# Kernel tuning notes

Measured on AMD Instinct MI355X. Metric: run time of the kernel, lower is better.

Reference implementation:

```python
import jax, jax.numpy as jnp
import numpy as np

LOTRI2MAT = np.array([[0, 1, 3], [1, 2, 4], [3, 4, 5]])  # lower-tri 6-vec -> symmetric 3x3
MAT2LOTRI_I = np.array([0, 1, 1, 2, 2, 2])
MAT2LOTRI_J = np.array([0, 0, 1, 0, 1, 2])


def trilinear_warp_border(img, ddf):
    """MONAI Warp(mode='bilinear', padding_mode='border', align_corners=True).
    img: (B,C,H,W,D), ddf: (B,3,H,W,D) displacement in voxel units.
    Samples img at x + ddf(x), clamping coords to the volume (border padding).
    """
    B, C, H, W, D = img.shape
    base = jnp.stack(
        jnp.meshgrid(jnp.arange(H), jnp.arange(W), jnp.arange(D), indexing='ij'),
        axis=0,
    ).astype(img.dtype)  # (3,H,W,D)
    coords = ddf + base[None]  # (B,3,H,W,D)
    x = jnp.clip(coords[:, 0], 0.0, H - 1)
    y = jnp.clip(coords[:, 1], 0.0, W - 1)
    z = jnp.clip(coords[:, 2], 0.0, D - 1)

    x0f, y0f, z0f = jnp.floor(x), jnp.floor(y), jnp.floor(z)
    fx, fy, fz = x - x0f, y - y0f, z - z0f
    x0 = jnp.clip(x0f.astype(jnp.int32), 0, H - 1)
    y0 = jnp.clip(y0f.astype(jnp.int32), 0, W - 1)
    z0 = jnp.clip(z0f.astype(jnp.int32), 0, D - 1)
    x1 = jnp.minimum(x0 + 1, H - 1)
    y1 = jnp.minimum(y0 + 1, W - 1)
    z1 = jnp.minimum(z0 + 1, D - 1)

    def gather(img_b, xi, yi, zi):
        flat = (xi * W + yi) * D + zi  # (H,W,D)
        return img_b.reshape(C, -1)[:, flat.reshape(-1)].reshape(C, H, W, D)

    g = jax.vmap(gather)  # over batch

    out = jnp.zeros_like(img)
    for xi, wx in ((x0, 1.0 - fx), (x1, fx)):
        for yi, wy in ((y0, 1.0 - fy), (y1, fy)):
            for zi, wz in ((z0, 1.0 - fz), (z1, fz)):
                out = out + g(img, xi, yi, zi) * (wx * wy * wz)[:, None]
    return out


def jacobian_of_ddf(ddf):
    """J = I + du/dx via central differences (one-sided at boundaries).
    ddf: (B,3,H,W,D) -> (B,H,W,D,3,3) with J[...,i,j] = d u_i / d x_j + delta_ij."""
    grads = jnp.gradient(ddf, axis=(2, 3, 4))  # list over j of (B,3,H,W,D)
    J = jnp.stack(grads, axis=2)  # (B,3(i),3(j),H,W,D)
    J = J + jnp.eye(3, dtype=ddf.dtype)[None, :, :, None, None, None]
    return jnp.transpose(J, (0, 3, 4, 5, 1, 2))  # (B,H,W,D,3,3)


def setup_inputs() -> dict:
    key = jax.random.key(0)
    k1, k2 = jax.random.split(key)
    dti = jax.random.normal(k1, (2, 6, 64, 64, 64), dtype=jnp.float32)
    ddf = jax.random.normal(k2, (2, 3, 64, 64, 64), dtype=jnp.float32)
    return {"dti": dti, "ddf": ddf}


def reference(dti, ddf):
    b, _, h, w, d = dti.shape
    # 1) trilinear warp of the 6-channel lower-tri DTI
    dti_warped = trilinear_warp_border(dti, ddf)  # (B,6,H,W,D)
    # 2) lower-tri -> full symmetric 3x3, spatial-last
    M = dti_warped[:, LOTRI2MAT]                      # (B,3,3,H,W,D)
    M = jnp.transpose(M, (0, 3, 4, 5, 1, 2))          # (B,H,W,D,3,3)
    # 3) Jacobian of the deformation and its polar-decomposition rotation (finite strain)
    J = jacobian_of_ddf(ddf)                          # (B,H,W,D,3,3)
    U, _, Vh = jnp.linalg.svd(J, full_matrices=False)
    R = jnp.matmul(U, Vh)                             # orthogonal factor of J
    # 4) rotate tensors: R^T M R
    out = jnp.einsum('...ji,...jk,...kl->...il', R, M, R)
    # 5) back to lower-tri channel-first form
    out = jnp.transpose(out, (0, 4, 5, 1, 2, 3))      # (B,3,3,H,W,D)
    return out[:, MAT2LOTRI_I, MAT2LOTRI_J]           # (B,6,H,W,D)
```

## Files before the change

kernel.cpp:

```cpp
#include <hip/hip_runtime.h>

#define NVOX 262144
#define TOTAL (2 * NVOX)

typedef float f2u __attribute__((ext_vector_type(2), aligned(4)));

__global__ void zero_count(int* __restrict__ bad) {
    if (threadIdx.x == 0) bad[0] = 0;
}

__global__ __launch_bounds__(256)
void warp_main(const float* __restrict__ dti,
               const float* __restrict__ ddf,
               float* __restrict__ out,
               int* __restrict__ bad, int max_bad)
{
    const int idx = blockIdx.x * 256 + threadIdx.x;
    const int b = idx >> 18;
    const int r = idx & (NVOX - 1);
    const int x = r >> 12;
    const int y = (r >> 6) & 63;
    const int z = r & 63;

    const float* db = ddf + (size_t)b * 3 * NVOX;

    const float ux = db[r];
    const float uy = db[NVOX + r];
    const float uz = db[2 * NVOX + r];

    const float cx = fminf(fmaxf((float)x + ux, 0.0f), 63.0f);
    const float cy = fminf(fmaxf((float)y + uy, 0.0f), 63.0f);
    const float cz = fminf(fmaxf((float)z + uz, 0.0f), 63.0f);
    const float fx0 = floorf(cx), fy0 = floorf(cy), fz0 = floorf(cz);
    const float fx = cx - fx0, fy = cy - fy0, fz = cz - fz0;
    const int x0 = (int)fx0, y0 = (int)fy0, z0 = (int)fz0;
    const int x1 = min(x0 + 1, 63), y1 = min(y0 + 1, 63);

    const float gx = 1.0f - fx, gy = 1.0f - fy, gz = 1.0f - fz;
    const float q00 = gx * gy, q01 = gx * fy, q10 = fx * gy, q11 = fx * fy;

    const bool ztop = (z0 == 63);
    const int zb = ztop ? 62 : z0;
    const int p00 = (x0 * 64 + y0) * 64 + zb, p01 = (x0 * 64 + y1) * 64 + zb;
    const int p10 = (x1 * 64 + y0) * 64 + zb, p11 = (x1 * 64 + y1) * 64 + zb;

    const float* tb = dti + (size_t)b * 6 * NVOX;
    float m[6];
#pragma unroll
    for (int c = 0; c < 6; ++c) {
        const float* tc = tb + c * NVOX;
        const f2u v00 = *(const f2u*)(tc + p00);
        const f2u v01 = *(const f2u*)(tc + p01);
        const f2u v10 = *(const f2u*)(tc + p10);
        const f2u v11 = *(const f2u*)(tc + p11);
        const float l00 = (ztop ? v00.y : v00.x) * gz + v00.y * fz;
        const float l01 = (ztop ? v01.y : v01.x) * gz + v01.y * fz;
        const float l10 = (ztop ? v10.y : v10.x) * gz + v10.y * fz;
        const float l11 = (ztop ? v11.y : v11.x) * gz + v11.y * fz;
        m[c] = q00 * l00 + q01 * l01 + q10 * l10 + q11 * l11;
    }

    const int xm = max(x - 1, 0), xp = min(x + 1, 63);
    const int ym = max(y - 1, 0), yp = min(y + 1, 63);
    const int zm = max(z - 1, 0), zp = min(z + 1, 63);
    const float sx = (xp - xm == 2) ? 0.5f : 1.0f;
    const float sy = (yp - ym == 2) ? 0.5f : 1.0f;
    const float sz = (zp - zm == 2) ? 0.5f : 1.0f;

    float P[3][3];
#pragma unroll
    for (int i = 0; i < 3; ++i) {
        const float* ui = db + i * NVOX;
        const float ctr = (i == 0) ? ux : (i == 1) ? uy : uz;
        P[i][0] = (ui[(xp * 64 + y) * 64 + z] - ui[(xm * 64 + y) * 64 + z]) * sx
                + (i == 0 ? 1.0f : 0.0f);
        P[i][1] = (ui[(x * 64 + yp) * 64 + z] - ui[(x * 64 + ym) * 64 + z]) * sy
                + (i == 1 ? 1.0f : 0.0f);
        P[i][2] = (__shfl(ctr, zp) - __shfl(ctr, zm)) * sz + (i == 2 ? 1.0f : 0.0f);
    }

    float cond_est = 0.0f;
#pragma unroll
    for (int it = 0; it < 6; ++it) {
        const float C00 = P[1][1] * P[2][2] - P[1][2] * P[2][1];
        const float C01 = P[1][2] * P[2][0] - P[1][0] * P[2][2];
        const float C02 = P[1][0] * P[2][1] - P[1][1] * P[2][0];
        const float C10 = P[0][2] * P[2][1] - P[0][1] * P[2][2];
        const float C11 = P[0][0] * P[2][2] - P[0][2] * P[2][0];
        const float C12 = P[0][1] * P[2][0] - P[0][0] * P[2][1];
        const float C20 = P[0][1] * P[1][2] - P[0][2] * P[1][1];
        const float C21 = P[0][2] * P[1][0] - P[0][0] * P[1][2];
        const float C22 = P[0][0] * P[1][1] - P[0][1] * P[1][0];
        const float det = P[0][0] * C00 + P[0][1] * C01 + P[0][2] * C02;

        const float n2 = P[0][0]*P[0][0] + P[0][1]*P[0][1] + P[0][2]*P[0][2]
                       + P[1][0]*P[1][0] + P[1][1]*P[1][1] + P[1][2]*P[1][2]
                       + P[2][0]*P[2][0] + P[2][1]*P[2][1] + P[2][2]*P[2][2];
        const float a2 = C00*C00 + C01*C01 + C02*C02
                       + C10*C10 + C11*C11 + C12*C12
                       + C20*C20 + C21*C21 + C22*C22;

        const float ad = fmaxf(fabsf(det), 1e-30f);
        if (it == 0) cond_est = sqrtf(n2 * a2) / ad;

        const float t  = fmaxf(sqrtf(a2 / n2), 1e-20f);
        const float sg = (det < 0.0f) ? -1.0f : 1.0f;
        const float c1 = 0.5f * sqrtf(t / ad);
        const float c2 = 0.5f * sg / sqrtf(t * ad);

        P[0][0] = c1 * P[0][0] + c2 * C00;  P[0][1] = c1 * P[0][1] + c2 * C01;  P[0][2] = c1 * P[0][2] + c2 * C02;
        P[1][0] = c1 * P[1][0] + c2 * C10;  P[1][1] = c1 * P[1][1] + c2 * C11;  P[1][2] = c1 * P[1][2] + c2 * C12;
        P[2][0] = c1 * P[2][0] + c2 * C20;  P[2][1] = c1 * P[2][1] + c2 * C21;  P[2][2] = c1 * P[2][2] + c2 * C22;
    }

    const float M3[3][3] = {{m[0], m[1], m[3]},
                            {m[1], m[2], m[4]},
                            {m[3], m[4], m[5]}};
    float T[3][3];
#pragma unroll
    for (int i = 0; i < 3; ++i)
#pragma unroll
        for (int j = 0; j < 3; ++j)
            T[i][j] = P[0][i] * M3[0][j] + P[1][i] * M3[1][j] + P[2][i] * M3[2][j];

    float A[3][3];
#pragma unroll
    for (int i = 0; i < 3; ++i)
#pragma unroll
        for (int j = 0; j < 3; ++j)
            A[i][j] = T[i][0] * P[0][j] + T[i][1] * P[1][j] + T[i][2] * P[2][j];

    float* ob = out + (size_t)b * 6 * NVOX;
    ob[0 * NVOX + r] = A[0][0];
    ob[1 * NVOX + r] = A[1][0];
    ob[2 * NVOX + r] = A[1][1];
    ob[3 * NVOX + r] = A[2][0];
    ob[4 * NVOX + r] = A[2][1];
    ob[5 * NVOX + r] = A[2][2];

    if (cond_est > 1e4f) {
        const int slot = atomicAdd(bad, 1);
        if (slot < max_bad) bad[1 + slot] = idx;
    }
}

__global__ __launch_bounds__(256)
void rescue(const float* __restrict__ dti,
            const float* __restrict__ ddf,
            float* __restrict__ out,
            const int* __restrict__ bad, int max_bad)
{
    const int n = min(bad[0], max_bad);
    for (int k = blockIdx.x * 256 + threadIdx.x; k < n; k += 4 * 256) {
        const int idx = bad[1 + k];
        const int b = idx >> 18;
        const int r = idx & (NVOX - 1);
        const int x = r >> 12;
        const int y = (r >> 6) & 63;
        const int z = r & 63;

        const float* db = ddf + (size_t)b * 3 * NVOX;

        const float cx = fminf(fmaxf((float)x + db[r], 0.0f), 63.0f);
        const float cy = fminf(fmaxf((float)y + db[NVOX + r], 0.0f), 63.0f);
        const float cz = fminf(fmaxf((float)z + db[2 * NVOX + r], 0.0f), 63.0f);
        const float fx0 = floorf(cx), fy0 = floorf(cy), fz0 = floorf(cz);
        const float fx = cx - fx0, fy = cy - fy0, fz = cz - fz0;
        const int x0 = (int)fx0, y0 = (int)fy0, z0 = (int)fz0;
        const int x1 = min(x0 + 1, 63), y1 = min(y0 + 1, 63), z1 = min(z0 + 1, 63);
        const float gx = 1.0f - fx, gy = 1.0f - fy, gz = 1.0f - fz;
        const float w000 = gx*gy*gz, w001 = gx*gy*fz, w010 = gx*fy*gz, w011 = gx*fy*fz;
        const float w100 = fx*gy*gz, w101 = fx*gy*fz, w110 = fx*fy*gz, w111 = fx*fy*fz;
        const int o000 = (x0*64+y0)*64+z0, o001 = (x0*64+y0)*64+z1;
        const int o010 = (x0*64+y1)*64+z0, o011 = (x0*64+y1)*64+z1;
        const int o100 = (x1*64+y0)*64+z0, o101 = (x1*64+y0)*64+z1;
        const int o110 = (x1*64+y1)*64+z0, o111 = (x1*64+y1)*64+z1;

        const float* tb = dti + (size_t)b * 6 * NVOX;
        float m[6];
        for (int c = 0; c < 6; ++c) {
            const float* tc = tb + c * NVOX;
            m[c] = w000*tc[o000] + w001*tc[o001] + w010*tc[o010] + w011*tc[o011]
                 + w100*tc[o100] + w101*tc[o101] + w110*tc[o110] + w111*tc[o111];
        }

        const int xm = max(x-1,0), xp = min(x+1,63);
        const int ym = max(y-1,0), yp = min(y+1,63);
        const int zm = max(z-1,0), zp = min(z+1,63);
        const double sx = (xp-xm==2)?0.5:1.0, sy = (yp-ym==2)?0.5:1.0, sz = (zp-zm==2)?0.5:1.0;
        double X[3][3];
        for (int i = 0; i < 3; ++i) {
            const float* ui = db + i * NVOX;
            X[i][0] = ((double)ui[(xp*64+y)*64+z] - (double)ui[(xm*64+y)*64+z]) * sx + (i==0?1.0:0.0);
            X[i][1] = ((double)ui[(x*64+yp)*64+z] - (double)ui[(x*64+ym)*64+z]) * sy + (i==1?1.0:0.0);
            X[i][2] = ((double)ui[(x*64+y)*64+zp] - (double)ui[(x*64+y)*64+zm]) * sz + (i==2?1.0:0.0);
        }

        for (int it = 0; it < 14; ++it) {
            double mx = 0.0;
            for (int i = 0; i < 3; ++i)
                for (int j = 0; j < 3; ++j) mx = fmax(mx, fabs(X[i][j]));
            const double s = 1.0 / fmax(mx, 1e-300);
            for (int i = 0; i < 3; ++i)
                for (int j = 0; j < 3; ++j) X[i][j] *= s;

            const double C00 = X[1][1]*X[2][2] - X[1][2]*X[2][1];
            const double C01 = X[1][2]*X[2][0] - X[1][0]*X[2][2];
            const double C02 = X[1][0]*X[2][1] - X[1][1]*X[2][0];
            const double C10 = X[0][2]*X[2][1] - X[0][1]*X[2][2];
            const double C11 = X[0][0]*X[2][2] - X[0][2]*X[2][0];
            const double C12 = X[0][1]*X[2][0] - X[0][0]*X[2][1];
            const double C20 = X[0][1]*X[1][2] - X[0][2]*X[1][1];
            const double C21 = X[0][2]*X[1][0] - X[0][0]*X[1][2];
            const double C22 = X[0][0]*X[1][1] - X[0][1]*X[1][0];
            const double det = X[0][0]*C00 + X[0][1]*C01 + X[0][2]*C02;
            const double n2 = X[0][0]*X[0][0]+X[0][1]*X[0][1]+X[0][2]*X[0][2]
                            + X[1][0]*X[1][0]+X[1][1]*X[1][1]+X[1][2]*X[1][2]
                            + X[2][0]*X[2][0]+X[2][1]*X[2][1]+X[2][2]*X[2][2];
            const double a2 = C00*C00+C01*C01+C02*C02 + C10*C10+C11*C11+C12*C12
                            + C20*C20+C21*C21+C22*C22;
            const double t  = fmax(sqrt(a2 / n2), 1e-150);
            const double ad = fmax(fabs(det), 1e-280);
            const double sg = (det < 0.0) ? -1.0 : 1.0;
            const double c1 = 0.5 * sqrt(t / ad);
            const double c2 = 0.5 * sg / sqrt(t * ad);
            X[0][0]=c1*X[0][0]+c2*C00; X[0][1]=c1*X[0][1]+c2*C01; X[0][2]=c1*X[0][2]+c2*C02;
            X[1][0]=c1*X[1][0]+c2*C10; X[1][1]=c1*X[1][1]+c2*C11; X[1][2]=c1*X[1][2]+c2*C12;
            X[2][0]=c1*X[2][0]+c2*C20; X[2][1]=c1*X[2][1]+c2*C21; X[2][2]=c1*X[2][2]+c2*C22;
        }

        const double M3[3][3] = {{(double)m[0], (double)m[1], (double)m[3]},
                                 {(double)m[1], (double)m[2], (double)m[4]},
                                 {(double)m[3], (double)m[4], (double)m[5]}};
        double T[3][3], A[3][3];
        for (int i = 0; i < 3; ++i)
            for (int j = 0; j < 3; ++j)
                T[i][j] = X[0][i]*M3[0][j] + X[1][i]*M3[1][j] + X[2][i]*M3[2][j];
        for (int i = 0; i < 3; ++i)
            for (int j = 0; j < 3; ++j)
                A[i][j] = T[i][0]*X[0][j] + T[i][1]*X[1][j] + T[i][2]*X[2][j];

        float* ob = out + (size_t)b * 6 * NVOX;
        ob[0 * NVOX + r] = (float)A[0][0];
        ob[1 * NVOX + r] = (float)A[1][0];
        ob[2 * NVOX + r] = (float)A[1][1];
        ob[3 * NVOX + r] = (float)A[2][0];
        ob[4 * NVOX + r] = (float)A[2][1];
        ob[5 * NVOX + r] = (float)A[2][2];
    }
}

extern "C" void kernel_launch(void* const* d_in, const int* in_sizes, int n_in,
                              void* d_out, int out_size, void* d_ws, size_t ws_size,
                              hipStream_t stream) {
    const float* dti = (const float*)d_in[0];
    const float* ddf = (const float*)d_in[1];
    float* out = (float*)d_out;
    int* bad = (int*)d_ws;
    const int max_bad = (int)min((size_t)8192, ws_size / 4 - 1);

    zero_count<<<1, 64, 0, stream>>>(bad);
    warp_main<<<TOTAL / 256, 256, 0, stream>>>(dti, ddf, out, bad, max_bad);
    rescue<<<4, 256, 0, stream>>>(dti, ddf, out, bad, max_bad);
}
```

Baseline: 108.2 us.

## Process two z-voxels per thread and flag ill-conditioned voxels with NaN

Each thread now handles two adjacent z voxels. It uses vectorized float2 loads for the ddf stencil and float2 stores for the output, and gets z-neighbours by shuffling across lanes. The atomic bad-voxel list and its zeroing kernel are removed. Ill-conditioned voxels are instead marked by writing a NaN into channel 0, and the rescue kernel now scans every voxel for that NaN marker across a full grid. This saves one launch and the atomics and halves the thread count, at the cost of a full-size rescue pass that reads channel 0 of the output, plus higher register pressure per thread.

```diff
diff --git a/kernel.cpp b/kernel.cpp
--- a/kernel.cpp
+++ b/kernel.cpp
@@ -1,36 +1,18 @@
 #include <hip/hip_runtime.h>
+#include <math.h>
 
 #define NVOX 262144
-#define TOTAL (2 * NVOX)
 
 typedef float f2u __attribute__((ext_vector_type(2), aligned(4)));
 
-__global__ void zero_count(int* __restrict__ bad) {
-    if (threadIdx.x == 0) bad[0] = 0;
-}
-
-__global__ __launch_bounds__(256)
-void warp_main(const float* __restrict__ dti,
-               const float* __restrict__ ddf,
-               float* __restrict__ out,
-               int* __restrict__ bad, int max_bad)
-{
-    const int idx = blockIdx.x * 256 + threadIdx.x;
-    const int b = idx >> 18;
-    const int r = idx & (NVOX - 1);
-    const int x = r >> 12;
-    const int y = (r >> 6) & 63;
-    const int z = r & 63;
-
-    const float* db = ddf + (size_t)b * 3 * NVOX;
-
-    const float ux = db[r];
-    const float uy = db[NVOX + r];
-    const float uz = db[2 * NVOX + r];
-
-    const float cx = fminf(fmaxf((float)x + ux, 0.0f), 63.0f);
-    const float cy = fminf(fmaxf((float)y + uy, 0.0f), 63.0f);
-    const float cz = fminf(fmaxf((float)z + uz, 0.0f), 63.0f);
+__device__ __forceinline__ void warp_m(const float* __restrict__ tb,
+                                       int xi, int yi, int zi,
+                                       float ux, float uy, float uz,
+                                       float m[6])
+{
+    const float cx = fminf(fmaxf((float)xi + ux, 0.0f), 63.0f);
+    const float cy = fminf(fmaxf((float)yi + uy, 0.0f), 63.0f);
+    const float cz = fminf(fmaxf((float)zi + uz, 0.0f), 63.0f);
     const float fx0 = floorf(cx), fy0 = floorf(cy), fz0 = floorf(cz);
     const float fx = cx - fx0, fy = cy - fy0, fz = cz - fz0;
     const int x0 = (int)fx0, y0 = (int)fy0, z0 = (int)fz0;
@@ -44,8 +26,6 @@
     const int p00 = (x0 * 64 + y0) * 64 + zb, p01 = (x0 * 64 + y1) * 64 + zb;
     const int p10 = (x1 * 64 + y0) * 64 + zb, p11 = (x1 * 64 + y1) * 64 + zb;
 
-    const float* tb = dti + (size_t)b * 6 * NVOX;
-    float m[6];
 #pragma unroll
     for (int c = 0; c < 6; ++c) {
         const float* tc = tb + c * NVOX;
@@ -59,26 +39,10 @@
         const float l11 = (ztop ? v11.y : v11.x) * gz + v11.y * fz;
         m[c] = q00 * l00 + q01 * l01 + q10 * l10 + q11 * l11;
     }
-
-    const int xm = max(x - 1, 0), xp = min(x + 1, 63);
-    const int ym = max(y - 1, 0), yp = min(y + 1, 63);
-    const int zm = max(z - 1, 0), zp = min(z + 1, 63);
-    const float sx = (xp - xm == 2) ? 0.5f : 1.0f;
-    const float sy = (yp - ym == 2) ? 0.5f : 1.0f;
-    const float sz = (zp - zm == 2) ? 0.5f : 1.0f;
-
-    float P[3][3];
-#pragma unroll
-    for (int i = 0; i < 3; ++i) {
-        const float* ui = db + i * NVOX;
-        const float ctr = (i == 0) ? ux : (i == 1) ? uy : uz;
-        P[i][0] = (ui[(xp * 64 + y) * 64 + z] - ui[(xm * 64 + y) * 64 + z]) * sx
-                + (i == 0 ? 1.0f : 0.0f);
-        P[i][1] = (ui[(x * 64 + yp) * 64 + z] - ui[(x * 64 + ym) * 64 + z]) * sy
-                + (i == 1 ? 1.0f : 0.0f);
-        P[i][2] = (__shfl(ctr, zp) - __shfl(ctr, zm)) * sz + (i == 2 ? 1.0f : 0.0f);
-    }
-
+}
+
+__device__ __forceinline__ float polar3(float P[3][3])
+{
     float cond_est = 0.0f;
 #pragma unroll
     for (int it = 0; it < 6; ++it) {
@@ -112,7 +76,12 @@
         P[1][0] = c1 * P[1][0] + c2 * C10;  P[1][1] = c1 * P[1][1] + c2 * C11;  P[1][2] = c1 * P[1][2] + c2 * C12;
         P[2][0] = c1 * P[2][0] + c2 * C20;  P[2][1] = c1 * P[2][1] + c2 * C21;  P[2][2] = c1 * P[2][2] + c2 * C22;
     }
-
+    return cond_est;
+}
+
+__device__ __forceinline__ void sandwich(const float P[3][3], const float m[6],
+                                         float A6[6])
+{
     const float M3[3][3] = {{m[0], m[1], m[3]},
                             {m[1], m[2], m[4]},
                             {m[3], m[4], m[5]}};
@@ -122,43 +91,100 @@
 #pragma unroll
         for (int j = 0; j < 3; ++j)
             T[i][j] = P[0][i] * M3[0][j] + P[1][i] * M3[1][j] + P[2][i] * M3[2][j];
-
-    float A[3][3];
-#pragma unroll
-    for (int i = 0; i < 3; ++i)
-#pragma unroll
-        for (int j = 0; j < 3; ++j)
-            A[i][j] = T[i][0] * P[0][j] + T[i][1] * P[1][j] + T[i][2] * P[2][j];
-
-    float* ob = out + (size_t)b * 6 * NVOX;
-    ob[0 * NVOX + r] = A[0][0];
-    ob[1 * NVOX + r] = A[1][0];
-    ob[2 * NVOX + r] = A[1][1];
-    ob[3 * NVOX + r] = A[2][0];
-    ob[4 * NVOX + r] = A[2][1];
-    ob[5 * NVOX + r] = A[2][2];
-
-    if (cond_est > 1e4f) {
-        const int slot = atomicAdd(bad, 1);
-        if (slot < max_bad) bad[1 + slot] = idx;
+    A6[0] = T[0][0]*P[0][0] + T[0][1]*P[1][0] + T[0][2]*P[2][0];
+    A6[1] = T[1][0]*P[0][0] + T[1][1]*P[1][0] + T[1][2]*P[2][0];
+    A6[2] = T[1][0]*P[0][1] + T[1][1]*P[1][1] + T[1][2]*P[2][1];
+    A6[3] = T[2][0]*P[0][0] + T[2][1]*P[1][0] + T[2][2]*P[2][0];
+    A6[4] = T[2][0]*P[0][1] + T[2][1]*P[1][1] + T[2][2]*P[2][1];
+    A6[5] = T[2][0]*P[0][2] + T[2][1]*P[1][2] + T[2][2]*P[2][2];
+}
+
+__global__ __launch_bounds__(256)
+void warp_main(const float* __restrict__ dti,
+               const float* __restrict__ ddf,
+               float* __restrict__ out)
+{
+    const int idx2 = blockIdx.x * 256 + threadIdx.x;
+    const int v0 = idx2 << 1;
+    const int b  = v0 >> 18;
+    const int r0 = v0 & (NVOX - 1);
+    const int x  = r0 >> 12;
+    const int y  = (r0 >> 6) & 63;
+    const int z0 = r0 & 63;
+    const int lane = threadIdx.x & 63;
+    const int k = lane & 31;
+
+    const float* db = ddf + (size_t)b * 3 * NVOX;
+
+    f2u uc[3];
+#pragma unroll
+    for (int i = 0; i < 3; ++i) uc[i] = *(const f2u*)(db + i * NVOX + r0);
+
+    const int xm = max(x - 1, 0), xp = min(x + 1, 63);
+    const int ym = max(y - 1, 0), yp = min(y + 1, 63);
+    const float sx = (xp - xm == 2) ? 0.5f : 1.0f;
+    const float sy = (yp - ym == 2) ? 0.5f : 1.0f;
+    const float sz0 = (k == 0) ? 1.0f : 0.5f;
+    const float sz1 = (k == 31) ? 1.0f : 0.5f;
+
+    float P0[3][3], P1[3][3];
+#pragma unroll
+    for (int i = 0; i < 3; ++i) {
+        const float* ui = db + i * NVOX;
+        const f2u vxp = *(const f2u*)(ui + (xp * 64 + y) * 64 + z0);
+        const f2u vxm = *(const f2u*)(ui + (xm * 64 + y) * 64 + z0);
+        const f2u vyp = *(const f2u*)(ui + (x * 64 + yp) * 64 + z0);
+        const f2u vym = *(const f2u*)(ui + (x * 64 + ym) * 64 + z0);
+        P0[i][0] = (vxp.x - vxm.x) * sx + (i == 0 ? 1.0f : 0.0f);
+        P1[i][0] = (vxp.y - vxm.y) * sx + (i == 0 ? 1.0f : 0.0f);
+        P0[i][1] = (vyp.x - vym.x) * sy + (i == 1 ? 1.0f : 0.0f);
+        P1[i][1] = (vyp.y - vym.y) * sy + (i == 1 ? 1.0f : 0.0f);
+        const float prev_y = __shfl(uc[i].y, (lane - 1) & 63);
+        const float next_x = __shfl(uc[i].x, (lane + 1) & 63);
+        const float zm0v = (k == 0)  ? uc[i].x : prev_y;
+        const float zp1v = (k == 31) ? uc[i].y : next_x;
+        P0[i][2] = (uc[i].y - zm0v) * sz0 + (i == 2 ? 1.0f : 0.0f);
+        P1[i][2] = (zp1v - uc[i].x) * sz1 + (i == 2 ? 1.0f : 0.0f);
+    }
+
+    const float* tb = dti + (size_t)b * 6 * NVOX;
+    float m0[6], m1[6];
+    warp_m(tb, x, y, z0,     uc[0].x, uc[1].x, uc[2].x, m0);
+    warp_m(tb, x, y, z0 + 1, uc[0].y, uc[1].y, uc[2].y, m1);
+
+    const float cond0 = polar3(P0);
+    const float cond1 = polar3(P1);
+
+    float A0[6], A1[6];
+    sandwich(P0, m0, A0);
+    sandwich(P1, m1, A1);
+
+    const float qnan = __int_as_float(0x7fc00000);
+    if (cond0 > 1e4f) A0[0] = qnan;
+    if (cond1 > 1e4f) A1[0] = qnan;
+
+    float* ob = out + (size_t)b * 6 * NVOX + r0;
+#pragma unroll
+    for (int c = 0; c < 6; ++c) {
+        f2u v; v.x = A0[c]; v.y = A1[c];
+        *(f2u*)(ob + c * NVOX) = v;
     }
 }
 
 __global__ __launch_bounds__(256)
 void rescue(const float* __restrict__ dti,
             const float* __restrict__ ddf,
-            float* __restrict__ out,
-            const int* __restrict__ bad, int max_bad)
-{
-    const int n = min(bad[0], max_bad);
-    for (int k = blockIdx.x * 256 + threadIdx.x; k < n; k += 4 * 256) {
-        const int idx = bad[1 + k];
-        const int b = idx >> 18;
-        const int r = idx & (NVOX - 1);
-        const int x = r >> 12;
-        const int y = (r >> 6) & 63;
-        const int z = r & 63;
-
+            float* __restrict__ out)
+{
+    const int t = blockIdx.x * 256 + threadIdx.x;
+#pragma unroll
+    for (int b = 0; b < 2; ++b) {
+        const int r = t;
+        float* ob = out + (size_t)b * 6 * NVOX;
+        const float v = ob[r];
+        if (!(v != v)) continue;
+
+        const int x = r >> 12, y = (r >> 6) & 63, z = r & 63;
         const float* db = ddf + (size_t)b * 3 * NVOX;
 
         const float cx = fminf(fmaxf((float)x + db[r], 0.0f), 63.0f);
@@ -219,11 +245,11 @@
                             + X[2][0]*X[2][0]+X[2][1]*X[2][1]+X[2][2]*X[2][2];
             const double a2 = C00*C00+C01*C01+C02*C02 + C10*C10+C11*C11+C12*C12
                             + C20*C20+C21*C21+C22*C22;
-            const double t  = fmax(sqrt(a2 / n2), 1e-150);
+            const double t2 = fmax(sqrt(a2 / n2), 1e-150);
             const double ad = fmax(fabs(det), 1e-280);
             const double sg = (det < 0.0) ? -1.0 : 1.0;
-            const double c1 = 0.5 * sqrt(t / ad);
-            const double c2 = 0.5 * sg / sqrt(t * ad);
+            const double c1 = 0.5 * sqrt(t2 / ad);
+            const double c2 = 0.5 * sg / sqrt(t2 * ad);
             X[0][0]=c1*X[0][0]+c2*C00; X[0][1]=c1*X[0][1]+c2*C01; X[0][2]=c1*X[0][2]+c2*C02;
             X[1][0]=c1*X[1][0]+c2*C10; X[1][1]=c1*X[1][1]+c2*C11; X[1][2]=c1*X[1][2]+c2*C12;
             X[2][0]=c1*X[2][0]+c2*C20; X[2][1]=c1*X[2][1]+c2*C21; X[2][2]=c1*X[2][2]+c2*C22;
@@ -240,7 +266,6 @@
             for (int j = 0; j < 3; ++j)
                 A[i][j] = T[i][0]*X[0][j] + T[i][1]*X[1][j] + T[i][2]*X[2][j];
 
-        float* ob = out + (size_t)b * 6 * NVOX;
         ob[0 * NVOX + r] = (float)A[0][0];
         ob[1 * NVOX + r] = (float)A[1][0];
         ob[2 * NVOX + r] = (float)A[1][1];
@@ -256,10 +281,6 @@
     const float* dti = (const float*)d_in[0];
     const float* ddf = (const float*)d_in[1];
     float* out = (float*)d_out;
-    int* bad = (int*)d_ws;
-    const int max_bad = (int)min((size_t)8192, ws_size / 4 - 1);
-
-    zero_count<<<1, 64, 0, stream>>>(bad);
-    warp_main<<<TOTAL / 256, 256, 0, stream>>>(dti, ddf, out, bad, max_bad);
-    rescue<<<4, 256, 0, stream>>>(dti, ddf, out, bad, max_bad);
-}
+    warp_main<<<NVOX / 256, 256, 0, stream>>>(dti, ddf, out);
+    rescue<<<NVOX / 256, 256, 0, stream>>>(dti, ddf, out);
+}
```

Measured after the change: 117.9 us. 8.9% more time.
